# Kernel tuning notes

Measured on AMD Instinct MI355X. Metric: run time of the kernel, lower is better.

Reference implementation:

```python
import jax, jax.numpy as jnp
import numpy as np

B, T, D_MODEL, STATE = 4, 4096, 1024, 256
LN_EPS = 1e-5


def setup_inputs() -> dict:
    key = jax.random.key(0)
    ks = jax.random.split(key, 8)
    x = jax.random.normal(ks[0], (B, T, D_MODEL), dtype=jnp.float32)
    bound_d = 1.0 / np.sqrt(D_MODEL)
    bound_n = 1.0 / np.sqrt(STATE)
    Wa_w = jax.random.normal(ks[1], (STATE, D_MODEL), dtype=jnp.float32) * 0.02
    Wa_b = jnp.zeros((STATE,), dtype=jnp.float32)
    WB_w = jax.random.normal(ks[2], (STATE, D_MODEL), dtype=jnp.float32) * 0.02
    WB_b = jax.random.uniform(ks[3], (STATE,), jnp.float32, -bound_d, bound_d)
    WC_w = jax.random.normal(ks[4], (D_MODEL, STATE), dtype=jnp.float32) * 0.02
    WC_b = jax.random.uniform(ks[5], (D_MODEL,), jnp.float32, -bound_n, bound_n)
    log_gamma = jnp.asarray(0.0, dtype=jnp.float32)
    D_skip = jax.random.normal(ks[6], (D_MODEL,), dtype=jnp.float32) * 0.01
    ln_w = jnp.ones((D_MODEL,), dtype=jnp.float32)
    ln_b = jnp.zeros((D_MODEL,), dtype=jnp.float32)
    return {"x": x, "Wa_w": Wa_w, "Wa_b": Wa_b, "log_gamma": log_gamma,
            "WB_w": WB_w, "WB_b": WB_b, "WC_w": WC_w, "WC_b": WC_b,
            "D_skip": D_skip, "ln_w": ln_w, "ln_b": ln_b}


def _layernorm(x, w, b):
    mu = jnp.mean(x, axis=-1, keepdims=True)
    var = jnp.mean(jnp.square(x - mu), axis=-1, keepdims=True)
    return (x - mu) * jax.lax.rsqrt(var + LN_EPS) * w + b


def reference(x, Wa_w, Wa_b, log_gamma, WB_w, WB_b, WC_w, WC_b, D_skip, ln_w, ln_b):
    residual = x
    xn = _layernorm(x, ln_w, ln_b)                      # (B,T,D)
    # Fourier eigenvalues: gamma * tanh(W_a x), FFT, magnitude-contracting scale
    gamma = jax.nn.sigmoid(log_gamma)
    a = gamma * jnp.tanh(jnp.einsum('btd,nd->btn', xn, Wa_w) + Wa_b)  # (B,T,n) real
    a_hat = jnp.fft.fft(a, axis=-1)                     # (B,T,n) complex, conj-symmetric
    mag = jnp.maximum(jnp.abs(a_hat), 1e-8)
    a_hat = a_hat * jax.nn.sigmoid(2.0 * (1.0 - mag))
    # Input projection in Fourier domain
    u = jnp.einsum('btd,nd->btn', xn, WB_w) + WB_b
    u_hat = jnp.fft.fft(u, axis=-1)                     # (B,T,n) complex
    # Linear recurrence h_t = a_t * h_{t-1} + b_t via associative scan over time
    def combine(c1, c2):
        a1, b1 = c1
        a2, b2 = c2
        return (a1 * a2, a2 * b1 + b2)
    _, h_hat = jax.lax.associative_scan(combine, (a_hat, u_hat), axis=1)
    h = jnp.real(jnp.fft.ifft(h_hat, axis=-1)).astype(x.dtype)        # (B,T,n)
    y = jnp.einsum('btn,dn->btd', h, WC_w) + WC_b + D_skip * residual
    return y
```

## Files before the change

### kernel.cpp

```cpp
#include <hip/hip_runtime.h>


typedef unsigned short ushort_t;
typedef short s16x8 __attribute__((ext_vector_type(8)));
typedef float f32x4 __attribute__((ext_vector_type(4)));
typedef _Float16 f16x8 __attribute__((ext_vector_type(8)));
typedef _Float16 f16x2 __attribute__((ext_vector_type(2)));

#define B_ 4
#define T_ 4096
#define D_ 1024
#define N_ 256
#define KB_ 129
#define M_ (B_*T_)

#define SWZ(i) ((i) ^ (((i) >> 3) & 6))

__device__ __forceinline__ ushort_t f2bf(float f) {
  unsigned u = __float_as_uint(f);
  u = (u + 0x7FFFu + ((u >> 16) & 1u)) >> 16;
  return (ushort_t)u;
}
__device__ __forceinline__ float2 cmul(float2 a, float2 b) {
  return make_float2(a.x*b.x - a.y*b.y, a.x*b.y + a.y*b.x);
}
__device__ __forceinline__ float fast_tanh(float x) {
  return 1.f - 2.f / (__expf(2.f * x) + 1.f);
}

typedef const __attribute__((address_space(1))) unsigned glb_u32;
typedef __attribute__((address_space(3))) unsigned lds_u32;
__device__ __forceinline__ void gload16(const void* g, void* l) {
  __builtin_amdgcn_global_load_lds((glb_u32*)g, (lds_u32*)l, 16, 0, 0);
}

__global__ __launch_bounds__(256) void ln_prep_kernel(const float* __restrict__ x,
    const float* __restrict__ w, const float* __restrict__ bb,
    ushort_t* __restrict__ xn,
    const float* __restrict__ Wa, const float* __restrict__ WB,
    const float* __restrict__ WC, ushort_t* __restrict__ Wab,
    ushort_t* __restrict__ WCb) {
  int tid = threadIdx.x;
  if (blockIdx.x >= 4096) {
    int i4 = ((blockIdx.x - 4096) * 256 + tid) * 4;
    float4 v;
    ushort_t* dst;
    if (i4 < 262144)        { v = *(const float4*)(Wa + i4);          dst = Wab + i4; }
    else if (i4 < 524288)   { v = *(const float4*)(WB + i4 - 262144); dst = Wab + i4; }
    else                    { v = *(const float4*)(WC + i4 - 524288); dst = WCb + i4 - 524288; }
    ushort4 o;
    o.x = f2bf(v.x); o.y = f2bf(v.y); o.z = f2bf(v.z); o.w = f2bf(v.w);
    *(ushort4*)dst = o;
    return;
  }
  int lane = tid & 63, wv = tid >> 6;
  int row = blockIdx.x * 4 + wv;
  const float4* xr = (const float4*)(x + (size_t)row * D_);
  float4 v[4];
  float s = 0.f, sq = 0.f;
  #pragma unroll
  for (int j = 0; j < 4; ++j) {
    v[j] = xr[lane + 64 * j];
    s  += v[j].x + v[j].y + v[j].z + v[j].w;
    sq += v[j].x*v[j].x + v[j].y*v[j].y + v[j].z*v[j].z + v[j].w*v[j].w;
  }
  #pragma unroll
  for (int off = 32; off >= 1; off >>= 1) {
    s  += __shfl_xor(s, off);
    sq += __shfl_xor(sq, off);
  }
  float mu  = s * (1.0f / D_);
  float var = sq * (1.0f / D_) - mu * mu;
  float rs  = rsqrtf(var + 1e-5f);
  const float4* w4 = (const float4*)w;
  const float4* b4 = (const float4*)bb;
  ushort4* o4 = (ushort4*)(xn + (size_t)row * D_);
  #pragma unroll
  for (int j = 0; j < 4; ++j) {
    float4 wv_ = w4[lane + 64 * j];
    float4 bv_ = b4[lane + 64 * j];
    ushort4 o;
    o.x = f2bf((v[j].x - mu) * rs * wv_.x + bv_.x);
    o.y = f2bf((v[j].y - mu) * rs * wv_.y + bv_.y);
    o.z = f2bf((v[j].z - mu) * rs * wv_.z + bv_.z);
    o.w = f2bf((v[j].w - mu) * rs * wv_.w + bv_.w);
    o4[lane + 64 * j] = o;
  }
}

template<bool EPI, int BN, bool HOUT>
__global__ __launch_bounds__(256) void gemm_bf16(
    const ushort_t* __restrict__ A, int lda,
    const ushort_t* __restrict__ B, int ldb,
    void* __restrict__ Cv, int ldc,
    int K, int ntiles,
    const float* __restrict__ bias,
    const float* __restrict__ dskip,
    const float* __restrict__ xres) {
  constexpr int NF = BN / 32;
  __shared__ ushort_t Alds[128 * 32];
  __shared__ ushort_t Blds[BN * 32];
  int bid = blockIdx.x;
  int cpx = gridDim.x >> 3;
  bid = (bid & 7) * cpx + (bid >> 3);
  int mt = bid / ntiles, nt = bid % ntiles;
  int m0 = mt * 128, n0 = nt * BN;
  int tid = threadIdx.x;
  int lane = tid & 63, wid = tid >> 6;
  int wm = wid >> 1, wn = wid & 1;

  int lrow = lane >> 2;
  int scol = (lane & 3) * 8;
  const ushort_t* gA0 = A + (size_t)(m0 + wid * 32 + lrow) * lda + scol;
  const ushort_t* gA1 = gA0 + (size_t)16 * lda;
  ushort_t* lA0 = &Alds[(wid * 32) * 32];
  ushort_t* lA1 = lA0 + 16 * 32;
  constexpr int BROWS = BN / 4;
  const ushort_t* gB0 = B + (size_t)(n0 + wid * BROWS + lrow) * ldb + scol;
  ushort_t* lB0 = &Blds[(wid * BROWS) * 32];

  f32x4 acc[4][NF] = {};
  int koff = (lane >> 4) * 8;
  int rbase = lane & 15;

  for (int k0 = 0; k0 < K; k0 += 32) {
    __syncthreads();
    gload16(gA0 + k0, lA0);
    gload16(gA1 + k0, lA1);
    gload16(gB0 + k0, lB0);
    if constexpr (BN == 128) gload16(gB0 + (size_t)16 * ldb + k0, lB0 + 16 * 32);
    __syncthreads();
    s16x8 af[4], bf[NF];
    #pragma unroll
    for (int i = 0; i < 4; ++i)
      af[i] = *reinterpret_cast<const s16x8*>(&Alds[(wm * 64 + i * 16 + rbase) * 32 + koff]);
    #pragma unroll
    for (int j = 0; j < NF; ++j)
      bf[j] = *reinterpret_cast<const s16x8*>(&Blds[(wn * (BN / 2) + j * 16 + rbase) * 32 + koff]);
    #pragma unroll
    for (int i = 0; i < 4; ++i)
      #pragma unroll
      for (int j = 0; j < NF; ++j)
        acc[i][j] = __builtin_amdgcn_mfma_f32_16x16x32_bf16(af[i], bf[j], acc[i][j], 0, 0, 0);
  }

  int r0 = (lane >> 4) * 4, cc = lane & 15;
  #pragma unroll
  for (int i = 0; i < 4; ++i) {
    #pragma unroll
    for (int j = 0; j < NF; ++j) {
      int col = n0 + wn * (BN / 2) + j * 16 + cc;
      #pragma unroll
      for (int r = 0; r < 4; ++r) {
        int row = m0 + wm * 64 + i * 16 + r0 + r;
        float v = acc[i][j][r];
        if constexpr (EPI) v += bias[col] + dskip[col] * xres[(size_t)row * ldc + col];
        if constexpr (HOUT) ((_Float16*)Cv)[(size_t)row * ldc + col] = (_Float16)v;
        else                ((float*)Cv)[(size_t)row * ldc + col] = v;
      }
    }
  }
}

__global__ __launch_bounds__(512) void fft_fwd(const _Float16* __restrict__ au,
    const float* __restrict__ ba, const float* __restrict__ bu,
    const float* __restrict__ lg, _Float16* __restrict__ ah, _Float16* __restrict__ uh) {
  __shared__ float2 Z[8][256];
  __shared__ float2 Tw[128];
  int tid = threadIdx.x;
  int m0 = blockIdx.x * 8;
  int tg = tid >> 6, lane = tid & 63;
  if (tid < 128) {
    float sn, cs;
    __sincosf(-3.14159265358979f / 128.f * (float)tid, &sn, &cs);
    Tw[SWZ(tid)] = make_float2(cs, sn);
  }
  float gamma = 1.f / (1.f + __expf(-lg[0]));
  const _Float16* row = au + (size_t)(m0 + tg) * (2 * N_);
  #pragma unroll
  for (int j = 0; j < 4; ++j) {
    int n = lane + 64 * j;
    float a = gamma * fast_tanh((float)row[n] + ba[n]);
    float u = (float)row[N_ + n] + bu[n];
    Z[tg][SWZ(__brev((unsigned)n) >> 24)] = make_float2(a, u);
  }
  __syncthreads();
  #pragma unroll
  for (int st = 1; st <= 8; ++st) {
    int half = 1 << (st - 1), shift = 8 - st;
    #pragma unroll
    for (int s = 0; s < 2; ++s) {
      int bi = lane + 64 * s;
      int j = bi & (half - 1);
      int i0 = ((bi & ~(half - 1)) << 1) | j;
      int i1 = i0 + half;
      float2 tw = Tw[SWZ(j << shift)];
      float2 z0 = Z[tg][SWZ(i0)], z1 = Z[tg][SWZ(i1)];
      float2 t = cmul(tw, z1);
      Z[tg][SWZ(i1)] = make_float2(z0.x - t.x, z0.y - t.y);
      Z[tg][SWZ(i0)] = make_float2(z0.x + t.x, z0.y + t.y);
    }
    __syncthreads();
  }
  int b = m0 >> 12, tb = m0 & (T_ - 1);
  #pragma unroll
  for (int p = 0; p < 3; ++p) {
    int k = (tid >> 3) + p * 64;
    int tl = tid & 7;
    if (k <= 128) {
      float2 zk = Z[tl][SWZ(k)];
      float2 zn = Z[tl][SWZ((256 - k) & 255)];
      float2 Af = make_float2(0.5f * (zk.x + zn.x), 0.5f * (zk.y - zn.y));
      float2 Uf = make_float2(0.5f * (zk.y + zn.y), -0.5f * (zk.x - zn.x));
      float mag = fmaxf(sqrtf(Af.x * Af.x + Af.y * Af.y), 1e-8f);
      float scl = 1.f / (1.f + __expf(-2.f * (1.f - mag)));
      Af.x *= scl; Af.y *= scl;
      size_t off2 = (((size_t)(b * KB_ + k)) * T_ + tb + tl) * 2;
      f16x2 av; av[0] = (_Float16)Af.x; av[1] = (_Float16)Af.y;
      f16x2 uv; uv[0] = (_Float16)Uf.x; uv[1] = (_Float16)Uf.y;
      *(f16x2*)(ah + off2) = av;
      *(f16x2*)(uh + off2) = uv;
    }
  }
}

__global__ __launch_bounds__(512) void scan_kernel(const _Float16* __restrict__ ah,
                                                   _Float16* __restrict__ uh) {
  __shared__ float4 wagg[8];
  int tid = threadIdx.x;
  int lane = tid & 63, wv = tid >> 6;
  size_t base = (size_t)blockIdx.x * T_ * 2;
  const f16x8* a8 = (const f16x8*)(ah + base);
  f16x8* u8 = (f16x8*)(uh + base);
  f16x8 Av[2], Uv[2];
  #pragma unroll
  for (int q = 0; q < 2; ++q) { Av[q] = a8[tid * 2 + q]; Uv[q] = u8[tid * 2 + q]; }
  float2 La[8], Lb[8];
  float2 ra = make_float2(1.f, 0.f), rb = make_float2(0.f, 0.f);
  #pragma unroll
  for (int e = 0; e < 8; ++e) {
    const int q = e >> 2, i = (e & 3) * 2;
    float2 a = make_float2((float)Av[q][i], (float)Av[q][i + 1]);
    float2 u = make_float2((float)Uv[q][i], (float)Uv[q][i + 1]);
    float2 t = cmul(a, rb);
    rb = make_float2(t.x + u.x, t.y + u.y);
    ra = cmul(ra, a);
    La[e] = ra; Lb[e] = rb;
  }
  #pragma unroll
  for (int off = 1; off < 64; off <<= 1) {
    float ax = __shfl_up(ra.x, off, 64), ay = __shfl_up(ra.y, off, 64);
    float bx = __shfl_up(rb.x, off, 64), by = __shfl_up(rb.y, off, 64);
    if (lane >= off) {
      float2 Ap = make_float2(ax, ay), Bp = make_float2(bx, by);
      float2 nB = cmul(ra, Bp);
      nB.x += rb.x; nB.y += rb.y;
      ra = cmul(Ap, ra);
      rb = nB;
    }
  }
  if (lane == 63) wagg[wv] = make_float4(ra.x, ra.y, rb.x, rb.y);
  __syncthreads();
  float2 Bw = make_float2(0.f, 0.f);
  for (int w0 = 0; w0 < wv; ++w0) {
    float4 g = wagg[w0];
    float2 gA = make_float2(g.x, g.y), gB = make_float2(g.z, g.w);
    Bw = cmul(gA, Bw);
    Bw.x += gB.x; Bw.y += gB.y;
  }
  float ax = __shfl_up(ra.x, 1, 64), ay = __shfl_up(ra.y, 1, 64);
  float bx = __shfl_up(rb.x, 1, 64), by = __shfl_up(rb.y, 1, 64);
  float2 Ae, Be;
  if (lane == 0) { Ae = make_float2(1.f, 0.f); Be = make_float2(0.f, 0.f); }
  else           { Ae = make_float2(ax, ay);   Be = make_float2(bx, by);   }
  float2 Pb = cmul(Ae, Bw);
  Pb.x += Be.x; Pb.y += Be.y;
  #pragma unroll
  for (int q = 0; q < 2; ++q) {
    f16x8 o;
    #pragma unroll
    for (int e2 = 0; e2 < 4; ++e2) {
      const int e = q * 4 + e2;
      float2 h = cmul(La[e], Pb);
      h.x += Lb[e].x; h.y += Lb[e].y;
      o[e2 * 2]     = (_Float16)h.x;
      o[e2 * 2 + 1] = (_Float16)h.y;
    }
    u8[tid * 2 + q] = o;
  }
}

__global__ __launch_bounds__(256) void ifft_kernel(const _Float16* __restrict__ hh,
                                                   ushort_t* __restrict__ hb) {
  __shared__ float2 Hraw[8][132];
  __shared__ float2 Wz[4][256];
  __shared__ float2 Tw[128];
  int tid = threadIdx.x;
  int m0 = blockIdx.x * 8;
  int b = m0 >> 12, tb = m0 & (T_ - 1);
  if (tid < 128) {
    float sn, cs;
    __sincosf(3.14159265358979f / 128.f * (float)tid, &sn, &cs);
    Tw[SWZ(tid)] = make_float2(cs, sn);
  }
  #pragma unroll
  for (int p = 0; p < 5; ++p) {
    int k = p * 32 + (tid >> 3), tl = tid & 7;
    if (k <= 128) {
      f16x2 hv = *(const f16x2*)(hh + (((size_t)(b * KB_ + k)) * T_ + tb + tl) * 2);
      Hraw[tl][k] = make_float2((float)hv[0], (float)hv[1]);
    }
  }
  __syncthreads();
  #pragma unroll
  for (int p = 0; p < 3; ++p) {
    int idx = p * 256 + tid;
    if (idx < 516) {
      int k = idx >> 2, pr = idx & 3;
      float2 h1 = Hraw[2 * pr][k], h2 = Hraw[2 * pr + 1][k];
      Wz[pr][SWZ(__brev((unsigned)k) >> 24)] = make_float2(h1.x - h2.y, h1.y + h2.x);
      if (k >= 1 && k <= 127)
        Wz[pr][SWZ(__brev((unsigned)(256 - k)) >> 24)] = make_float2(h1.x + h2.y, h2.x - h1.y);
    }
  }
  __syncthreads();
  int pr = tid >> 6, lane = tid & 63;
  #pragma unroll
  for (int st = 1; st <= 8; ++st) {
    int half = 1 << (st - 1), shift = 8 - st;
    #pragma unroll
    for (int s = 0; s < 2; ++s) {
      int bi = lane + 64 * s;
      int j = bi & (half - 1);
      int i0 = ((bi & ~(half - 1)) << 1) | j;
      int i1 = i0 + half;
      float2 tw = Tw[SWZ(j << shift)];
      float2 z0 = Wz[pr][SWZ(i0)], z1 = Wz[pr][SWZ(i1)];
      float2 t = cmul(tw, z1);
      Wz[pr][SWZ(i1)] = make_float2(z0.x - t.x, z0.y - t.y);
      Wz[pr][SWZ(i0)] = make_float2(z0.x + t.x, z0.y + t.y);
    }
    __syncthreads();
  }
  const float inv = 1.f / 256.f;
  #pragma unroll
  for (int j = 0; j < 4; ++j) {
    int n = lane + 64 * j;
    float2 wv = Wz[pr][SWZ(n)];
    hb[(size_t)(m0 + 2 * pr) * N_ + n]     = f2bf(wv.x * inv);
    hb[(size_t)(m0 + 2 * pr + 1) * N_ + n] = f2bf(wv.y * inv);
  }
}

extern "C" void kernel_launch(void* const* d_in, const int* in_sizes, int n_in,
                              void* d_out, int out_size, void* d_ws, size_t ws_size,
                              hipStream_t stream) {
  const float* x      = (const float*)d_in[0];
  const float* Wa_w   = (const float*)d_in[1];
  const float* Wa_b   = (const float*)d_in[2];
  const float* lg     = (const float*)d_in[3];
  const float* WB_w   = (const float*)d_in[4];
  const float* WB_b   = (const float*)d_in[5];
  const float* WC_w   = (const float*)d_in[6];
  const float* WC_b   = (const float*)d_in[7];
  const float* D_skip = (const float*)d_in[8];
  const float* ln_w   = (const float*)d_in[9];
  const float* ln_b   = (const float*)d_in[10];
  float* out = (float*)d_out;
  char* ws = (char*)d_ws;

  ushort_t*  xn  = (ushort_t*)(ws + 0);
  ushort_t*  Wab = (ushort_t*)(ws + 33554432);
  ushort_t*  WCb = (ushort_t*)(ws + 34603008);
  _Float16*  au  = (_Float16*)(ws + 35127296);
  ushort_t*  hb  = (ushort_t*)(ws + 35127296);
  _Float16*  ah  = (_Float16*)(ws + 0);
  _Float16*  uh  = (_Float16*)(ws + 16908288);

  ln_prep_kernel<<<4864, 256, 0, stream>>>(x, ln_w, ln_b, xn,
                                           Wa_w, WB_w, WC_w, Wab, WCb);
  gemm_bf16<false, 64, true><<<1024, 256, 0, stream>>>(xn, D_, Wab, D_, au, 512,
                                                       D_, 8, nullptr, nullptr, nullptr);
  fft_fwd<<<M_ / 8, 512, 0, stream>>>(au, Wa_b, WB_b, lg, ah, uh);
  scan_kernel<<<B_ * KB_, 512, 0, stream>>>(ah, uh);
  ifft_kernel<<<M_ / 8, 256, 0, stream>>>(uh, hb);
  gemm_bf16<true, 128, false><<<1024, 256, 0, stream>>>(hb, N_, WCb, N_, out, D_,
                                                        N_, 8, WC_b, D_skip, x);
}
```

Before: 121.2 us.

## Double GEMM K-tile to 64 with XOR-swizzled LDS layout

The bf16 GEMM main loop now stages a K-slice of 64 instead of 32 per iteration, halving the number of barrier pairs and global-to-LDS rounds. Each thread loads 16-byte chunks with an XOR swizzle on the column index, and the MFMA fragment reads apply the matching swizzle to avoid LDS bank conflicts on the wider 128-byte rows. LDS use per block doubles, which may reduce occupancy, and K must be a multiple of 64.

Result: faster. 113.3 us (-6.6%).

```diff
diff --git a/kernel.cpp b/kernel.cpp
--- a/kernel.cpp
+++ b/kernel.cpp
@@ -98,8 +98,8 @@
     const float* __restrict__ dskip,
     const float* __restrict__ xres) {
   constexpr int NF = BN / 32;
-  __shared__ ushort_t Alds[128 * 32];
-  __shared__ ushort_t Blds[BN * 32];
+  __shared__ ushort_t Alds[128 * 64];
+  __shared__ ushort_t Blds[BN * 64];
   int bid = blockIdx.x;
   int cpx = gridDim.x >> 3;
   bid = (bid & 7) * cpx + (bid >> 3);
@@ -109,39 +109,44 @@
   int lane = tid & 63, wid = tid >> 6;
   int wm = wid >> 1, wn = wid & 1;
 
-  int lrow = lane >> 2;
-  int scol = (lane & 3) * 8;
-  const ushort_t* gA0 = A + (size_t)(m0 + wid * 32 + lrow) * lda + scol;
-  const ushort_t* gA1 = gA0 + (size_t)16 * lda;
-  ushort_t* lA0 = &Alds[(wid * 32) * 32];
-  ushort_t* lA1 = lA0 + 16 * 32;
+  int lr8 = lane >> 3;
+  int gd  = (lane & 7) ^ lr8;
+  const ushort_t* gA = A + (size_t)(m0 + wid * 32 + lr8) * lda + gd * 8;
+  ushort_t* lA = &Alds[(wid * 32) * 64];
   constexpr int BROWS = BN / 4;
-  const ushort_t* gB0 = B + (size_t)(n0 + wid * BROWS + lrow) * ldb + scol;
-  ushort_t* lB0 = &Blds[(wid * BROWS) * 32];
+  const ushort_t* gB = B + (size_t)(n0 + wid * BROWS + lr8) * ldb + gd * 8;
+  ushort_t* lB = &Blds[(wid * BROWS) * 64];
 
   f32x4 acc[4][NF] = {};
-  int koff = (lane >> 4) * 8;
   int rbase = lane & 15;
-
-  for (int k0 = 0; k0 < K; k0 += 32) {
+  int rb7 = lane & 7;
+  int gk0 = lane >> 4;
+
+  for (int k0 = 0; k0 < K; k0 += 64) {
     __syncthreads();
-    gload16(gA0 + k0, lA0);
-    gload16(gA1 + k0, lA1);
-    gload16(gB0 + k0, lB0);
-    if constexpr (BN == 128) gload16(gB0 + (size_t)16 * ldb + k0, lB0 + 16 * 32);
+    #pragma unroll
+    for (int c = 0; c < 4; ++c)
+      gload16(gA + (size_t)(c * 8) * lda + k0, lA + c * 8 * 64);
+    #pragma unroll
+    for (int c = 0; c < BROWS / 8; ++c)
+      gload16(gB + (size_t)(c * 8) * ldb + k0, lB + c * 8 * 64);
     __syncthreads();
-    s16x8 af[4], bf[NF];
-    #pragma unroll
-    for (int i = 0; i < 4; ++i)
-      af[i] = *reinterpret_cast<const s16x8*>(&Alds[(wm * 64 + i * 16 + rbase) * 32 + koff]);
-    #pragma unroll
-    for (int j = 0; j < NF; ++j)
-      bf[j] = *reinterpret_cast<const s16x8*>(&Blds[(wn * (BN / 2) + j * 16 + rbase) * 32 + koff]);
-    #pragma unroll
-    for (int i = 0; i < 4; ++i)
+    #pragma unroll
+    for (int kk = 0; kk < 2; ++kk) {
+      int sl = ((gk0 + kk * 4) ^ rb7) * 8;
+      s16x8 af[4], bf[NF];
+      #pragma unroll
+      for (int i = 0; i < 4; ++i)
+        af[i] = *reinterpret_cast<const s16x8*>(&Alds[(wm * 64 + i * 16 + rbase) * 64 + sl]);
       #pragma unroll
       for (int j = 0; j < NF; ++j)
-        acc[i][j] = __builtin_amdgcn_mfma_f32_16x16x32_bf16(af[i], bf[j], acc[i][j], 0, 0, 0);
+        bf[j] = *reinterpret_cast<const s16x8*>(&Blds[(wn * (BN / 2) + j * 16 + rbase) * 64 + sl]);
+      #pragma unroll
+      for (int i = 0; i < 4; ++i)
+        #pragma unroll
+        for (int j = 0; j < NF; ++j)
+          acc[i][j] = __builtin_amdgcn_mfma_f32_16x16x32_bf16(af[i], bf[j], acc[i][j], 0, 0, 0);
+    }
   }
 
   int r0 = (lane >> 4) * 4, cc = lane & 15;
```
